# Kernel tuning notes

Hardware: AMD Instinct MI355X
Metric: run time of the kernel (lower is better)

Reference implementation:

```python
import jax, jax.numpy as jnp
import numpy as np

# Model dims (match init_kwargs)
B, S, H = 1, 2048, 1024
E = 16            # n_routed_experts
I = 768           # moe_intermediate_size
TOPK = 4          # num_experts_per_tok
G = 4             # n_group
TOPK_G = 2        # topk_group
SCALE = 2.5       # routed_scaling_factor
N_SHARED = 1      # n_shared_experts


def setup_inputs() -> dict:
    key = jax.random.key(0)
    ks = jax.random.split(key, 9)
    def rn(k, shape, scale=0.02):
        return jax.random.normal(k, shape, dtype=jnp.float32) * scale
    return dict(
        hidden_states=jax.random.normal(ks[0], (B, S, H), dtype=jnp.float32),
        gate_w=rn(ks[1], (E, H)),
        gate_bias=jax.random.normal(ks[2], (E,), dtype=jnp.float32) * 0.1,
        w1=rn(ks[3], (E, I, H)),   # gate_proj weights [out,in]
        w2=rn(ks[4], (E, H, I)),   # down_proj weights
        w3=rn(ks[5], (E, I, H)),   # up_proj weights
        ws1=rn(ks[6], (I * N_SHARED, H)),
        ws2=rn(ks[7], (H, I * N_SHARED)),
        ws3=rn(ks[8], (I * N_SHARED, H)),
    )


def _route(x, gate_w, gate_bias):
    """noaux_tc routing: sigmoid scores + bias, group top-k, top_k experts."""
    n = x.shape[0]
    logits = jnp.einsum('nh,eh->ne', x.astype(jnp.float32), gate_w)  # [N,E]
    scores = jax.nn.sigmoid(logits)
    sb = scores + gate_bias                                          # biased scores
    # group score = sum of top-2 biased scores in each group
    gs = sb.reshape(n, G, E // G)
    group_scores = jnp.sum(jax.lax.top_k(gs, 2)[0], axis=-1)         # [N,G]
    _, gidx = jax.lax.top_k(group_scores, TOPK_G)                    # [N,TOPK_G]
    gmask = jnp.sum(jax.nn.one_hot(gidx, G, dtype=sb.dtype), axis=1) # [N,G]
    emask = jnp.repeat(gmask, E // G, axis=-1)                       # [N,E]
    masked = jnp.where(emask > 0, sb, -jnp.inf)
    _, tidx = jax.lax.top_k(masked, TOPK)                            # [N,TOPK]
    w = jnp.take_along_axis(scores, tidx, axis=1)                    # unbiased weights
    w = w / (jnp.sum(w, axis=-1, keepdims=True) + 1e-20)             # norm_topk_prob
    return tidx, w * SCALE


def reference(hidden_states, gate_w, gate_bias, w1, w2, w3, ws1, ws2, ws3):
    b, s, h = hidden_states.shape
    x = hidden_states.reshape(-1, h)                                 # [N,H]
    tidx, tw = _route(x, gate_w, gate_bias)
    n = x.shape[0]
    # dense combine weights [N,E] (zero for unselected experts)
    combine = jnp.zeros((n, E), x.dtype).at[jnp.arange(n)[:, None], tidx].add(tw)
    # grouped SwiGLU experts (dense-over-experts reference form)
    g = jnp.einsum('nh,eih->nei', x, w1)
    u = jnp.einsum('nh,eih->nei', x, w3)
    hact = jax.nn.silu(g) * u * combine[:, :, None]
    y = jnp.einsum('nei,ehi->nh', hact, w2)
    # shared expert SwiGLU
    shared = jnp.einsum('ni,hi->nh', jax.nn.silu(x @ ws1.T) * (x @ ws3.T), ws2)
    return (y + shared).reshape(b, s, h)
```

## Files before the change

kernel.cpp:

```cpp
#include <hip/hip_runtime.h>
#include <hip/hip_bf16.h>
#include <math.h>

#define N_TOK 2048
#define H_DIM 1024
#define N_EXP 16
#define I_DIM 768
#define TOPK 4
#define SCALE 2.5f
#define MAX_TILES 96

typedef __attribute__((ext_vector_type(8))) short bf16x8;
typedef __attribute__((ext_vector_type(4))) float f32x4;

#define OFF_COUNTS   0
#define OFF_OFFSETS  128
#define OFF_TILES    256
#define OFF_TOKIDS   768
#define OFF_TOKW     (OFF_TOKIDS + N_EXP*N_TOK*4)
#define OFF_XB       (OFF_TOKW + N_EXP*N_TOK*4)
#define OFF_HACT     (OFF_XB + (size_t)N_TOK*H_DIM*2)
#define OFF_WB1      (OFF_HACT + (size_t)N_TOK*(TOPK+1)*I_DIM*2)
#define OFF_WB2      (OFF_WB1 + (size_t)N_EXP*I_DIM*H_DIM*2)
#define OFF_WB3      (OFF_WB2 + (size_t)N_EXP*H_DIM*I_DIM*2)
#define OFF_WSB1     (OFF_WB3 + (size_t)N_EXP*I_DIM*H_DIM*2)
#define OFF_WSB2     (OFF_WSB1 + (size_t)I_DIM*H_DIM*2)
#define OFF_WSB3     (OFF_WSB2 + (size_t)H_DIM*I_DIM*2)
#define OFF_GWT      (OFF_WSB3 + (size_t)I_DIM*H_DIM*2)

__device__ __forceinline__ ushort f2bf(float f) {
    union { __hip_bfloat16 h; ushort u; } cv;
    cv.h = __float2bfloat16(f);
    return cv.u;
}
__device__ __forceinline__ unsigned pack2(float lo, float hi) {
    return (unsigned)f2bf(lo) | ((unsigned)f2bf(hi) << 16);
}
__device__ __forceinline__ void async_copy16(const void* g, void* l) {
    __builtin_amdgcn_global_load_lds(
        (const __attribute__((address_space(1))) unsigned int*)g,
        (__attribute__((address_space(3))) unsigned int*)l, 16, 0, 0);
}

struct WcArgs {
    const float* src[7];
    ushort* dst[7];
    int n4[7];
};
__global__ void k_wconv(WcArgs a) {
    int id = blockIdx.y;
    const float4* s = (const float4*)a.src[id];
    uint2* d = (uint2*)a.dst[id];
    int n4 = a.n4[id];
    int stride = gridDim.x * 256;
    for (int i = blockIdx.x * 256 + threadIdx.x; i < n4; i += stride) {
        float4 v = s[i];
        uint2 p;
        p.x = pack2(v.x, v.y);
        p.y = pack2(v.z, v.w);
        d[i] = p;
    }
}

__global__ void k_gwt(const float* __restrict__ gw, float* __restrict__ gwT) {
    int i = blockIdx.x * 256 + threadIdx.x;
    int k = i >> 4, e = i & 15;
    gwT[i] = gw[e * H_DIM + k];
}

__launch_bounds__(256)
__global__ void k_route(const float* __restrict__ x, const float* __restrict__ gwT,
                        const float* __restrict__ gb,
                        int* __restrict__ counts, int* __restrict__ tok_ids,
                        float* __restrict__ tok_w) {
    __shared__ float lgs[4][N_EXP + 1];
    int tid = threadIdx.x;
    int wv = tid >> 6, lane = tid & 63;
    int e = lane & 15, ks = lane >> 4;
    int n = blockIdx.x * 4 + wv;

    const float* xr = x + (size_t)n * H_DIM + ks * 256;
    const float* wr = gwT + ks * 256 * N_EXP + e;
    float a0 = 0.f, a1 = 0.f, a2 = 0.f, a3 = 0.f;
#pragma unroll 8
    for (int k = 0; k < 256; k += 4) {
        float4 xv = *(const float4*)(xr + k);
        a0 += xv.x * wr[(k + 0) * N_EXP];
        a1 += xv.y * wr[(k + 1) * N_EXP];
        a2 += xv.z * wr[(k + 2) * N_EXP];
        a3 += xv.w * wr[(k + 3) * N_EXP];
    }
    float acc = (a0 + a1) + (a2 + a3);
    acc += __shfl_xor(acc, 16);
    acc += __shfl_xor(acc, 32);
    if (lane < 16) lgs[wv][lane] = acc;
    __syncthreads();

    if (tid < 4) {
        int n2 = blockIdx.x * 4 + tid;
        float sc[N_EXP], sb[N_EXP];
        for (int ee = 0; ee < N_EXP; ee++) {
            float l = lgs[tid][ee];
            sc[ee] = 1.f / (1.f + expf(-l));
            sb[ee] = sc[ee] + gb[ee];
        }
        float gsc[4];
        for (int g = 0; g < 4; g++) {
            float m1 = -1e30f, m2 = -1e30f;
            for (int j = 0; j < 4; j++) {
                float v = sb[4 * g + j];
                if (v > m1) { m2 = m1; m1 = v; }
                else if (v > m2) m2 = v;
            }
            gsc[g] = m1 + m2;
        }
        int g1 = 0;
        for (int g = 1; g < 4; g++) if (gsc[g] > gsc[g1]) g1 = g;
        int g2 = -1;
        for (int g = 0; g < 4; g++) {
            if (g == g1) continue;
            if (g2 < 0 || gsc[g] > gsc[g2]) g2 = g;
        }
        bool allowed[N_EXP];
        for (int ee = 0; ee < N_EXP; ee++) {
            int grp = ee >> 2;
            allowed[ee] = (grp == g1) || (grp == g2);
        }
        int chosen[TOPK];
        float wsum = 0.f;
        for (int k = 0; k < TOPK; k++) {
            int best = -1;
            for (int ee = 0; ee < N_EXP; ee++) {
                if (!allowed[ee]) continue;
                if (best < 0 || sb[ee] > sb[best]) best = ee;
            }
            chosen[k] = best;
            allowed[best] = false;
            wsum += sc[best];
        }
        float inv = SCALE / (wsum + 1e-20f);
        for (int k = 0; k < TOPK; k++) {
            int ee = chosen[k];
            int p = atomicAdd(&counts[ee], 1);
            tok_ids[ee * N_TOK + p] = n2;
            tok_w[ee * N_TOK + p] = sc[ee] * inv;
        }
    }
}

__global__ void k_scan(const int* __restrict__ counts, int* __restrict__ offsets,
                       int* __restrict__ tiles) {
    if (threadIdx.x == 0 && blockIdx.x == 0) {
        int off = 0;
        for (int e = 0; e < N_EXP; e++) { offsets[e] = off; off += counts[e]; }
        offsets[N_EXP] = off;
        int t = 0;
        for (int e = 0; e < N_EXP; e++)
            for (int m0 = 0; m0 < counts[e]; m0 += 128)
                tiles[t++] = e | ((m0 >> 7) << 5);
        for (int m0 = 0; m0 < N_TOK; m0 += 128)
            tiles[t++] = N_EXP | ((m0 >> 7) << 5);
        for (; t < MAX_TILES; t++) tiles[t] = -1;
    }
}

__launch_bounds__(256, 4)
__global__ void k_gateup(const ushort* __restrict__ xb, const ushort* __restrict__ wb1,
                         const ushort* __restrict__ wb3, const ushort* __restrict__ wsb1,
                         const ushort* __restrict__ wsb3, const int* __restrict__ counts,
                         const int* __restrict__ offsets, const int* __restrict__ tiles,
                         const int* __restrict__ tok_ids, const float* __restrict__ tok_w,
                         ushort* __restrict__ hact) {
    int desc = tiles[blockIdx.x];
    if (desc < 0) return;
    int e = desc & 31;
    int m0 = (desc >> 5) * 128;
    int i0 = blockIdx.y * 64;
    int Me = (e == N_EXP) ? N_TOK : counts[e];
    const ushort* W1 = (e == N_EXP) ? wsb1 : wb1 + (size_t)e * I_DIM * H_DIM;
    const ushort* W3 = (e == N_EXP) ? wsb3 : wb3 + (size_t)e * I_DIM * H_DIM;
    int base = offsets[e];

    __shared__ ushort As[128][64];
    __shared__ ushort Bs[128][64];
    __shared__ float tws[128];

    int tid = threadIdx.x;
    int wv = tid >> 6, lane = tid & 63;
    int seg = lane & 7, rsub = lane >> 3;
    int gch = (seg ^ rsub) * 8;

    if (tid < 128) {
        int r = m0 + tid;
        tws[tid] = (e == N_EXP) ? 1.f : ((r < Me) ? tok_w[e * N_TOK + r] : 0.f);
    }

    const ushort* aptr[4];
#pragma unroll
    for (int j = 0; j < 4; j++) {
        int gr = m0 + wv * 32 + j * 8 + rsub;
        int tok = (e == N_EXP) ? gr : ((gr < Me) ? tok_ids[e * N_TOK + gr] : 0);
        aptr[j] = xb + (size_t)tok * H_DIM + gch;
    }
    const ushort* bptr[4];
#pragma unroll
    for (int j = 0; j < 4; j++) {
        int r = wv * 32 + j * 8 + rsub;
        const ushort* W = (r < 64) ? (W1 + (size_t)(i0 + r) * H_DIM)
                                   : (W3 + (size_t)(i0 + r - 64) * H_DIM);
        bptr[j] = W + gch;
    }

    int quad = lane >> 4, lr = lane & 15, rx = lr & 7;
    f32x4 acc[2][8] = {};

    const int NK = H_DIM / 64;
    for (int k = 0; k < NK; k++) {
        int off = k * 64;
#pragma unroll
        for (int j = 0; j < 4; j++) async_copy16(aptr[j] + off, &As[wv * 32 + j * 8][0]);
#pragma unroll
        for (int j = 0; j < 4; j++) async_copy16(bptr[j] + off, &Bs[wv * 32 + j * 8][0]);
        __syncthreads();
#pragma unroll
        for (int ks = 0; ks < 2; ks++) {
            int co = ((ks * 4 + quad) ^ rx) * 8;
            bf16x8 a0 = *(const bf16x8*)&As[wv * 32 + lr][co];
            bf16x8 a1 = *(const bf16x8*)&As[wv * 32 + 16 + lr][co];
#pragma unroll
            for (int ni = 0; ni < 8; ni++) {
                bf16x8 bf = *(const bf16x8*)&Bs[ni * 16 + lr][co];
                acc[0][ni] = __builtin_amdgcn_mfma_f32_16x16x32_bf16(a0, bf, acc[0][ni], 0, 0, 0);
                acc[1][ni] = __builtin_amdgcn_mfma_f32_16x16x32_bf16(a1, bf, acc[1][ni], 0, 0, 0);
            }
        }
        __syncthreads();
    }

#pragma unroll
    for (int mi = 0; mi < 2; mi++) {
#pragma unroll
        for (int ni = 0; ni < 4; ni++) {
            f32x4 g = acc[mi][ni];
            f32x4 u = acc[mi][ni + 4];
#pragma unroll
            for (int rg = 0; rg < 4; rg++) {
                int ml = wv * 32 + mi * 16 + quad * 4 + rg;
                int row = m0 + ml;
                if (row < Me) {
                    float gg = g[rg], uu = u[rg];
                    float act = (gg / (1.f + expf(-gg))) * uu * tws[ml];
                    hact[(size_t)(base + row) * I_DIM + i0 + ni * 16 + lr] = f2bf(act);
                }
            }
        }
    }
}

__launch_bounds__(256, 4)
__global__ void k_down(const ushort* __restrict__ hact, const ushort* __restrict__ wb2,
                       const ushort* __restrict__ wsb2, const int* __restrict__ counts,
                       const int* __restrict__ offsets, const int* __restrict__ tiles,
                       const int* __restrict__ tok_ids, float* __restrict__ out) {
    int desc = tiles[blockIdx.x];
    if (desc < 0) return;
    int e = desc & 31;
    int m0 = (desc >> 5) * 128;
    int h0 = blockIdx.y * 128;
    int Me = (e == N_EXP) ? N_TOK : counts[e];
    const ushort* W2 = (e == N_EXP) ? wsb2 : wb2 + (size_t)e * H_DIM * I_DIM;
    int base = offsets[e];

    __shared__ ushort As[128][64];
    __shared__ ushort Bs[128][64];
    __shared__ int toks[128];

    int tid = threadIdx.x;
    int wv = tid >> 6, lane = tid & 63;
    int seg = lane & 7, rsub = lane >> 3;
    int gch = (seg ^ rsub) * 8;

    if (tid < 128) {
        int r = m0 + tid;
        toks[tid] = (e == N_EXP) ? r : ((r < Me) ? tok_ids[e * N_TOK + r] : 0);
    }

    const ushort* aptr[4];
#pragma unroll
    for (int j = 0; j < 4; j++) {
        int row = wv * 32 + j * 8 + rsub;
        aptr[j] = hact + (size_t)(base + m0 + row) * I_DIM + gch;
    }
    const ushort* bptr[4];
#pragma unroll
    for (int j = 0; j < 4; j++) {
        int r = wv * 32 + j * 8 + rsub;
        bptr[j] = W2 + (size_t)(h0 + r) * I_DIM + gch;
    }

    int quad = lane >> 4, lr = lane & 15, rx = lr & 7;
    f32x4 acc[2][8] = {};

    const int NK = I_DIM / 64;
    for (int k = 0; k < NK; k++) {
        int off = k * 64;
#pragma unroll
        for (int j = 0; j < 4; j++) async_copy16(aptr[j] + off, &As[wv * 32 + j * 8][0]);
#pragma unroll
        for (int j = 0; j < 4; j++) async_copy16(bptr[j] + off, &Bs[wv * 32 + j * 8][0]);
        __syncthreads();
#pragma unroll
        for (int ks = 0; ks < 2; ks++) {
            int co = ((ks * 4 + quad) ^ rx) * 8;
            bf16x8 a0 = *(const bf16x8*)&As[wv * 32 + lr][co];
            bf16x8 a1 = *(const bf16x8*)&As[wv * 32 + 16 + lr][co];
#pragma unroll
            for (int ni = 0; ni < 8; ni++) {
                bf16x8 bf = *(const bf16x8*)&Bs[ni * 16 + lr][co];
                acc[0][ni] = __builtin_amdgcn_mfma_f32_16x16x32_bf16(a0, bf, acc[0][ni], 0, 0, 0);
                acc[1][ni] = __builtin_amdgcn_mfma_f32_16x16x32_bf16(a1, bf, acc[1][ni], 0, 0, 0);
            }
        }
        __syncthreads();
    }

#pragma unroll
    for (int mi = 0; mi < 2; mi++) {
#pragma unroll
        for (int ni = 0; ni < 8; ni++) {
#pragma unroll
            for (int rg = 0; rg < 4; rg++) {
                int ml = wv * 32 + mi * 16 + quad * 4 + rg;
                int row = m0 + ml;
                if (row < Me) {
                    int tok = toks[ml];
                    atomicAdd(&out[(size_t)tok * H_DIM + h0 + ni * 16 + lr],
                              acc[mi][ni][rg]);
                }
            }
        }
    }
}

extern "C" void kernel_launch(void* const* d_in, const int* in_sizes, int n_in,
                              void* d_out, int out_size, void* d_ws, size_t ws_size,
                              hipStream_t stream) {
    const float* x   = (const float*)d_in[0];
    const float* gw  = (const float*)d_in[1];
    const float* gb  = (const float*)d_in[2];
    const float* w1  = (const float*)d_in[3];
    const float* w2  = (const float*)d_in[4];
    const float* w3  = (const float*)d_in[5];
    const float* ws1 = (const float*)d_in[6];
    const float* ws2 = (const float*)d_in[7];
    const float* ws3 = (const float*)d_in[8];
    float* out = (float*)d_out;

    char* wsb = (char*)d_ws;
    int* counts   = (int*)(wsb + OFF_COUNTS);
    int* offsets  = (int*)(wsb + OFF_OFFSETS);
    int* tiles    = (int*)(wsb + OFF_TILES);
    int* tok_ids  = (int*)(wsb + OFF_TOKIDS);
    float* tok_w  = (float*)(wsb + OFF_TOKW);
    ushort* xb    = (ushort*)(wsb + OFF_XB);
    ushort* hact  = (ushort*)(wsb + OFF_HACT);
    ushort* wb1   = (ushort*)(wsb + OFF_WB1);
    ushort* wb2   = (ushort*)(wsb + OFF_WB2);
    ushort* wb3   = (ushort*)(wsb + OFF_WB3);
    ushort* wsb1  = (ushort*)(wsb + OFF_WSB1);
    ushort* wsb2  = (ushort*)(wsb + OFF_WSB2);
    ushort* wsb3  = (ushort*)(wsb + OFF_WSB3);
    float* gwT    = (float*)(wsb + OFF_GWT);

    hipMemsetAsync(wsb, 0, 128, stream);
    hipMemsetAsync(d_out, 0, (size_t)out_size * 4, stream);

    WcArgs wa;
    wa.src[0] = w1;  wa.dst[0] = wb1;  wa.n4[0] = N_EXP * I_DIM * H_DIM / 4;
    wa.src[1] = w2;  wa.dst[1] = wb2;  wa.n4[1] = N_EXP * H_DIM * I_DIM / 4;
    wa.src[2] = w3;  wa.dst[2] = wb3;  wa.n4[2] = N_EXP * I_DIM * H_DIM / 4;
    wa.src[3] = ws1; wa.dst[3] = wsb1; wa.n4[3] = I_DIM * H_DIM / 4;
    wa.src[4] = ws2; wa.dst[4] = wsb2; wa.n4[4] = H_DIM * I_DIM / 4;
    wa.src[5] = ws3; wa.dst[5] = wsb3; wa.n4[5] = I_DIM * H_DIM / 4;
    wa.src[6] = x;   wa.dst[6] = xb;   wa.n4[6] = N_TOK * H_DIM / 4;
    k_wconv<<<dim3(3072, 7), 256, 0, stream>>>(wa);

    k_gwt<<<N_EXP * H_DIM / 256, 256, 0, stream>>>(gw, gwT);
    k_route<<<N_TOK / 4, 256, 0, stream>>>(x, gwT, gb, counts, tok_ids, tok_w);
    k_scan<<<1, 1, 0, stream>>>(counts, offsets, tiles);
    {
        dim3 grid(MAX_TILES, I_DIM / 64);
        k_gateup<<<grid, 256, 0, stream>>>(xb, wb1, wb3, wsb1, wsb3, counts, offsets,
                                           tiles, tok_ids, tok_w, hact);
    }
    {
        dim3 grid(MAX_TILES, H_DIM / 128);
        k_down<<<grid, 256, 0, stream>>>(hact, wb2, wsb2, counts, offsets, tiles,
                                         tok_ids, out);
    }
}
```

Measured before the change: 360.4 us.

## Fuse fp32-to-bf16 weight conversion into expert GEMM B-tile loads

Removes the separate whole-weight bf16 conversion pass and has the gate/up and down GEMM kernels read fp32 weights directly. Each kernel converts them to bf16 in registers and stores them into the shared-memory B tile, prefetching the next K slice into registers one iteration ahead. This avoids writing and re-reading a bf16 copy of all expert weights. In exchange, each tile re-reads fp32 weights (twice the bytes) across token tiles, and occupancy drops to 3 blocks per CU.

```diff
diff --git a/kernel.cpp b/kernel.cpp
--- a/kernel.cpp
+++ b/kernel.cpp
@@ -20,13 +20,7 @@
 #define OFF_TOKW     (OFF_TOKIDS + N_EXP*N_TOK*4)
 #define OFF_XB       (OFF_TOKW + N_EXP*N_TOK*4)
 #define OFF_HACT     (OFF_XB + (size_t)N_TOK*H_DIM*2)
-#define OFF_WB1      (OFF_HACT + (size_t)N_TOK*(TOPK+1)*I_DIM*2)
-#define OFF_WB2      (OFF_WB1 + (size_t)N_EXP*I_DIM*H_DIM*2)
-#define OFF_WB3      (OFF_WB2 + (size_t)N_EXP*H_DIM*I_DIM*2)
-#define OFF_WSB1     (OFF_WB3 + (size_t)N_EXP*I_DIM*H_DIM*2)
-#define OFF_WSB2     (OFF_WSB1 + (size_t)I_DIM*H_DIM*2)
-#define OFF_WSB3     (OFF_WSB2 + (size_t)H_DIM*I_DIM*2)
-#define OFF_GWT      (OFF_WSB3 + (size_t)I_DIM*H_DIM*2)
+#define OFF_GWT      (OFF_HACT + (size_t)N_TOK*(TOPK+1)*I_DIM*2)
 
 __device__ __forceinline__ ushort f2bf(float f) {
     union { __hip_bfloat16 h; ushort u; } cv;
@@ -42,24 +36,13 @@
         (__attribute__((address_space(3))) unsigned int*)l, 16, 0, 0);
 }
 
-struct WcArgs {
-    const float* src[7];
-    ushort* dst[7];
-    int n4[7];
-};
-__global__ void k_wconv(WcArgs a) {
-    int id = blockIdx.y;
-    const float4* s = (const float4*)a.src[id];
-    uint2* d = (uint2*)a.dst[id];
-    int n4 = a.n4[id];
-    int stride = gridDim.x * 256;
-    for (int i = blockIdx.x * 256 + threadIdx.x; i < n4; i += stride) {
-        float4 v = s[i];
-        uint2 p;
-        p.x = pack2(v.x, v.y);
-        p.y = pack2(v.z, v.w);
-        d[i] = p;
-    }
+__global__ void k_xconv(const float* __restrict__ x, ushort* __restrict__ xb) {
+    int i = blockIdx.x * 256 + threadIdx.x;
+    float4 v = ((const float4*)x)[i];
+    uint2 p;
+    p.x = pack2(v.x, v.y);
+    p.y = pack2(v.z, v.w);
+    ((uint2*)xb)[i] = p;
 }
 
 __global__ void k_gwt(const float* __restrict__ gw, float* __restrict__ gwT) {
@@ -164,10 +147,10 @@
     }
 }
 
-__launch_bounds__(256, 4)
-__global__ void k_gateup(const ushort* __restrict__ xb, const ushort* __restrict__ wb1,
-                         const ushort* __restrict__ wb3, const ushort* __restrict__ wsb1,
-                         const ushort* __restrict__ wsb3, const int* __restrict__ counts,
+__launch_bounds__(256, 3)
+__global__ void k_gateup(const ushort* __restrict__ xb, const float* __restrict__ w1,
+                         const float* __restrict__ w3, const float* __restrict__ ws1,
+                         const float* __restrict__ ws3, const int* __restrict__ counts,
                          const int* __restrict__ offsets, const int* __restrict__ tiles,
                          const int* __restrict__ tok_ids, const float* __restrict__ tok_w,
                          ushort* __restrict__ hact) {
@@ -177,8 +160,8 @@
     int m0 = (desc >> 5) * 128;
     int i0 = blockIdx.y * 64;
     int Me = (e == N_EXP) ? N_TOK : counts[e];
-    const ushort* W1 = (e == N_EXP) ? wsb1 : wb1 + (size_t)e * I_DIM * H_DIM;
-    const ushort* W3 = (e == N_EXP) ? wsb3 : wb3 + (size_t)e * I_DIM * H_DIM;
+    const float* W1 = (e == N_EXP) ? ws1 : w1 + (size_t)e * I_DIM * H_DIM;
+    const float* W3 = (e == N_EXP) ? ws3 : w3 + (size_t)e * I_DIM * H_DIM;
     int base = offsets[e];
 
     __shared__ ushort As[128][64];
@@ -202,25 +185,45 @@
         int tok = (e == N_EXP) ? gr : ((gr < Me) ? tok_ids[e * N_TOK + gr] : 0);
         aptr[j] = xb + (size_t)tok * H_DIM + gch;
     }
-    const ushort* bptr[4];
+    const float* bptrf[4];
 #pragma unroll
     for (int j = 0; j < 4; j++) {
         int r = wv * 32 + j * 8 + rsub;
-        const ushort* W = (r < 64) ? (W1 + (size_t)(i0 + r) * H_DIM)
-                                   : (W3 + (size_t)(i0 + r - 64) * H_DIM);
-        bptr[j] = W + gch;
+        const float* W = (r < 64) ? (W1 + (size_t)(i0 + r) * H_DIM)
+                                  : (W3 + (size_t)(i0 + r - 64) * H_DIM);
+        bptrf[j] = W + gch;
     }
 
     int quad = lane >> 4, lr = lane & 15, rx = lr & 7;
     f32x4 acc[2][8] = {};
 
     const int NK = H_DIM / 64;
+    float4 bv0[4], bv1[4];
+#pragma unroll
+    for (int j = 0; j < 4; j++) {
+        bv0[j] = *(const float4*)(bptrf[j]);
+        bv1[j] = *(const float4*)(bptrf[j] + 4);
+    }
     for (int k = 0; k < NK; k++) {
         int off = k * 64;
 #pragma unroll
         for (int j = 0; j < 4; j++) async_copy16(aptr[j] + off, &As[wv * 32 + j * 8][0]);
 #pragma unroll
-        for (int j = 0; j < 4; j++) async_copy16(bptr[j] + off, &Bs[wv * 32 + j * 8][0]);
+        for (int j = 0; j < 4; j++) {
+            uint4 p;
+            p.x = pack2(bv0[j].x, bv0[j].y);
+            p.y = pack2(bv0[j].z, bv0[j].w);
+            p.z = pack2(bv1[j].x, bv1[j].y);
+            p.w = pack2(bv1[j].z, bv1[j].w);
+            *(uint4*)&Bs[wv * 32 + j * 8 + rsub][seg * 8] = p;
+        }
+        if (k + 1 < NK) {
+#pragma unroll
+            for (int j = 0; j < 4; j++) {
+                bv0[j] = *(const float4*)(bptrf[j] + off + 64);
+                bv1[j] = *(const float4*)(bptrf[j] + off + 68);
+            }
+        }
         __syncthreads();
 #pragma unroll
         for (int ks = 0; ks < 2; ks++) {
@@ -257,9 +260,9 @@
     }
 }
 
-__launch_bounds__(256, 4)
-__global__ void k_down(const ushort* __restrict__ hact, const ushort* __restrict__ wb2,
-                       const ushort* __restrict__ wsb2, const int* __restrict__ counts,
+__launch_bounds__(256, 3)
+__global__ void k_down(const ushort* __restrict__ hact, const float* __restrict__ w2,
+                       const float* __restrict__ ws2, const int* __restrict__ counts,
                        const int* __restrict__ offsets, const int* __restrict__ tiles,
                        const int* __restrict__ tok_ids, float* __restrict__ out) {
     int desc = tiles[blockIdx.x];
@@ -268,7 +271,7 @@
     int m0 = (desc >> 5) * 128;
     int h0 = blockIdx.y * 128;
     int Me = (e == N_EXP) ? N_TOK : counts[e];
-    const ushort* W2 = (e == N_EXP) ? wsb2 : wb2 + (size_t)e * H_DIM * I_DIM;
+    const float* W2 = (e == N_EXP) ? ws2 : w2 + (size_t)e * H_DIM * I_DIM;
     int base = offsets[e];
 
     __shared__ ushort As[128][64];
@@ -291,23 +294,43 @@
         int row = wv * 32 + j * 8 + rsub;
         aptr[j] = hact + (size_t)(base + m0 + row) * I_DIM + gch;
     }
-    const ushort* bptr[4];
+    const float* bptrf[4];
 #pragma unroll
     for (int j = 0; j < 4; j++) {
         int r = wv * 32 + j * 8 + rsub;
-        bptr[j] = W2 + (size_t)(h0 + r) * I_DIM + gch;
+        bptrf[j] = W2 + (size_t)(h0 + r) * I_DIM + gch;
     }
 
     int quad = lane >> 4, lr = lane & 15, rx = lr & 7;
     f32x4 acc[2][8] = {};
 
     const int NK = I_DIM / 64;
+    float4 bv0[4], bv1[4];
+#pragma unroll
+    for (int j = 0; j < 4; j++) {
+        bv0[j] = *(const float4*)(bptrf[j]);
+        bv1[j] = *(const float4*)(bptrf[j] + 4);
+    }
     for (int k = 0; k < NK; k++) {
         int off = k * 64;
 #pragma unroll
         for (int j = 0; j < 4; j++) async_copy16(aptr[j] + off, &As[wv * 32 + j * 8][0]);
 #pragma unroll
-        for (int j = 0; j < 4; j++) async_copy16(bptr[j] + off, &Bs[wv * 32 + j * 8][0]);
+        for (int j = 0; j < 4; j++) {
+            uint4 p;
+            p.x = pack2(bv0[j].x, bv0[j].y);
+            p.y = pack2(bv0[j].z, bv0[j].w);
+            p.z = pack2(bv1[j].x, bv1[j].y);
+            p.w = pack2(bv1[j].z, bv1[j].w);
+            *(uint4*)&Bs[wv * 32 + j * 8 + rsub][seg * 8] = p;
+        }
+        if (k + 1 < NK) {
+#pragma unroll
+            for (int j = 0; j < 4; j++) {
+                bv0[j] = *(const float4*)(bptrf[j] + off + 64);
+                bv1[j] = *(const float4*)(bptrf[j] + off + 68);
+            }
+        }
         __syncthreads();
 #pragma unroll
         for (int ks = 0; ks < 2; ks++) {
@@ -364,38 +387,23 @@
     float* tok_w  = (float*)(wsb + OFF_TOKW);
     ushort* xb    = (ushort*)(wsb + OFF_XB);
     ushort* hact  = (ushort*)(wsb + OFF_HACT);
-    ushort* wb1   = (ushort*)(wsb + OFF_WB1);
-    ushort* wb2   = (ushort*)(wsb + OFF_WB2);
-    ushort* wb3   = (ushort*)(wsb + OFF_WB3);
-    ushort* wsb1  = (ushort*)(wsb + OFF_WSB1);
-    ushort* wsb2  = (ushort*)(wsb + OFF_WSB2);
-    ushort* wsb3  = (ushort*)(wsb + OFF_WSB3);
     float* gwT    = (float*)(wsb + OFF_GWT);
 
     hipMemsetAsync(wsb, 0, 128, stream);
     hipMemsetAsync(d_out, 0, (size_t)out_size * 4, stream);
 
-    WcArgs wa;
-    wa.src[0] = w1;  wa.dst[0] = wb1;  wa.n4[0] = N_EXP * I_DIM * H_DIM / 4;
-    wa.src[1] = w2;  wa.dst[1] = wb2;  wa.n4[1] = N_EXP * H_DIM * I_DIM / 4;
-    wa.src[2] = w3;  wa.dst[2] = wb3;  wa.n4[2] = N_EXP * I_DIM * H_DIM / 4;
-    wa.src[3] = ws1; wa.dst[3] = wsb1; wa.n4[3] = I_DIM * H_DIM / 4;
-    wa.src[4] = ws2; wa.dst[4] = wsb2; wa.n4[4] = H_DIM * I_DIM / 4;
-    wa.src[5] = ws3; wa.dst[5] = wsb3; wa.n4[5] = I_DIM * H_DIM / 4;
-    wa.src[6] = x;   wa.dst[6] = xb;   wa.n4[6] = N_TOK * H_DIM / 4;
-    k_wconv<<<dim3(3072, 7), 256, 0, stream>>>(wa);
-
+    k_xconv<<<N_TOK * H_DIM / 4 / 256, 256, 0, stream>>>(x, xb);
     k_gwt<<<N_EXP * H_DIM / 256, 256, 0, stream>>>(gw, gwT);
     k_route<<<N_TOK / 4, 256, 0, stream>>>(x, gwT, gb, counts, tok_ids, tok_w);
     k_scan<<<1, 1, 0, stream>>>(counts, offsets, tiles);
     {
         dim3 grid(MAX_TILES, I_DIM / 64);
-        k_gateup<<<grid, 256, 0, stream>>>(xb, wb1, wb3, wsb1, wsb3, counts, offsets,
+        k_gateup<<<grid, 256, 0, stream>>>(xb, w1, w3, ws1, ws3, counts, offsets,
                                            tiles, tok_ids, tok_w, hact);
     }
     {
         dim3 grid(MAX_TILES, H_DIM / 128);
-        k_down<<<grid, 256, 0, stream>>>(hact, wb2, wsb2, counts, offsets, tiles,
+        k_down<<<grid, 256, 0, stream>>>(hact, w2, ws2, counts, offsets, tiles,
                                          tok_ids, out);
     }
 }
```

New measurement: 364.7 us. Within noise of the previous version (+1.2%).
